# Performance work log

Measured on AMD Instinct MI355X. Metric: run time of the kernel, lower is better.

Reference implementation:

```python
import jax, jax.numpy as jnp
import numpy as np

N = 400000
CIN = 16
COUT = 32
K = 9  # taps in a (1,3,3) or (3,1,3) kernel
EPS = 1e-5


def subm_conv(feat, nbr, W):
    """Submanifold sparse conv as gather-matmul-scatter.
    feat: [N, C]; nbr: [N, K] indices in [0, N] (N == missing -> zero); W: [K, C, O].
    """
    feat_pad = jnp.concatenate([feat, jnp.zeros((1, feat.shape[1]), feat.dtype)], axis=0)
    g = feat_pad[nbr]                       # [N, K, C] irregular gather
    return jnp.einsum('nkc,kco->no', g, W)  # [N, O]


def bn_relu(x, gamma, beta, mean, var):
    # eval-mode BatchNorm1d over channel dim + ReLU
    return jax.nn.relu((x - mean) * jax.lax.rsqrt(var + EPS) * gamma + beta)


def setup_inputs() -> dict:
    key = jax.random.key(0)
    ks = jax.random.split(key, 8)
    features = jax.random.normal(ks[0], (N, CIN), jnp.float32)
    nbr13 = jax.random.randint(ks[1], (N, K), 0, N + 1, jnp.int32)
    nbr31 = jax.random.randint(ks[2], (N, K), 0, N + 1, jnp.int32)
    w1 = jax.random.normal(ks[3], (K, CIN, COUT), jnp.float32) * 0.05
    w12 = jax.random.normal(ks[4], (K, COUT, COUT), jnp.float32) * 0.05
    w2 = jax.random.normal(ks[5], (K, CIN, COUT), jnp.float32) * 0.05
    w3 = jax.random.normal(ks[6], (K, COUT, COUT), jnp.float32) * 0.05
    gamma = jax.random.uniform(ks[7], (4, COUT), jnp.float32, 0.5, 1.5)
    beta = jnp.zeros((4, COUT), jnp.float32)
    mean = jnp.zeros((4, COUT), jnp.float32)
    var = jnp.ones((4, COUT), jnp.float32)
    return dict(features=features, nbr13=nbr13, nbr31=nbr31,
                w1=w1, w12=w12, w2=w2, w3=w3,
                gamma=gamma, beta=beta, mean=mean, var=var)


def reference(features, nbr13, nbr31, w1, w12, w2, w3, gamma, beta, mean, var):
    # shortcut branch: conv1x3 -> BN -> ReLU -> conv3x1 -> BN -> ReLU
    sc = bn_relu(subm_conv(features, nbr13, w1), gamma[0], beta[0], mean[0], var[0])
    sc = bn_relu(subm_conv(sc, nbr31, w12), gamma[1], beta[1], mean[1], var[1])
    # main branch: conv3x1 -> BN -> ReLU -> conv1x3 -> BN -> ReLU
    out = bn_relu(subm_conv(features, nbr31, w2), gamma[2], beta[2], mean[2], var[2])
    out = bn_relu(subm_conv(out, nbr13, w3), gamma[3], beta[3], mean[3], var[3])
    return out + sc
```

## Files before the change

### kernel.cpp

```cpp
#include <hip/hip_runtime.h>

#define NPTS 400000
#define KTAPS 9
#define BN_EPS 1e-5f
#define NTILES (NPTS / 16)

typedef __attribute__((ext_vector_type(8))) short bf16x8;
typedef __attribute__((ext_vector_type(4))) float f32x4;

__device__ __forceinline__ unsigned short f2bf(float f) {
    union { float f; unsigned int i; } v; v.f = f;
    v.i += 0x7fffu + ((v.i >> 16) & 1u);
    return (unsigned short)(v.i >> 16);
}

__global__ __launch_bounds__(256) void cvt_feat(const float* __restrict__ feat,
                                                unsigned short* __restrict__ fb) {
    int n = blockIdx.x * 256 + threadIdx.x;
    if (n >= NPTS) return;
    const float4* p = reinterpret_cast<const float4*>(feat + (size_t)n * 16);
    float4 a = p[0], b = p[1], c = p[2], d = p[3];
    float v[16] = {a.x,a.y,a.z,a.w, b.x,b.y,b.z,b.w,
                   c.x,c.y,c.z,c.w, d.x,d.y,d.z,d.w};
    unsigned int pk[8];
    #pragma unroll
    for (int j = 0; j < 8; ++j)
        pk[j] = (unsigned int)f2bf(v[2*j]) | ((unsigned int)f2bf(v[2*j+1]) << 16);
    uint4* o = reinterpret_cast<uint4*>(fb + (size_t)n * 16);
    o[0] = make_uint4(pk[0], pk[1], pk[2], pk[3]);
    o[1] = make_uint4(pk[4], pk[5], pk[6], pk[7]);
}

__global__ __launch_bounds__(256) void pack_all(
    const float* __restrict__ w1, const float* __restrict__ w2,
    const float* __restrict__ w12, const float* __restrict__ w3,
    const float* __restrict__ gamma, const float* __restrict__ beta,
    const float* __restrict__ mean, const float* __restrict__ var,
    unsigned short* __restrict__ pw, float* __restrict__ sbf)
{
    int t = blockIdx.x * 256 + threadIdx.x;
    if (t < 28672) {
        const float* W; int CIN, f;
        if      (t < 5120)  { W = w1;  CIN = 16; f = t; }
        else if (t < 10240) { W = w2;  CIN = 16; f = t - 5120; }
        else if (t < 19456) { W = w12; CIN = 32; f = t - 10240; }
        else                { W = w3;  CIN = 32; f = t - 19456; }
        int j = f & 7, l = (f >> 3) & 63, fb = f >> 9;
        int g = fb >> 1, b = fb & 1;
        int kk = 8 * (l >> 4) + j;
        int tap, ch;
        if (CIN == 16) { tap = 2 * g + (kk >> 4); ch = kk & 15; }
        else           { tap = g;                 ch = kk;      }
        float w = (tap < KTAPS) ? W[((size_t)(tap * CIN + ch)) * 32 + b * 16 + (l & 15)] : 0.f;
        pw[t] = f2bf(w);
    } else if (t < 28672 + 128) {
        int r = t - 28672;
        float s  = gamma[r] * rsqrtf(var[r] + BN_EPS);
        float bb = beta[r] - mean[r] * s;
        sbf[2 * r]     = s;
        sbf[2 * r + 1] = bb;
    }
}

template<int CIN, bool ADD, bool OUT_BF16>
__global__ __launch_bounds__(256) void conv_mfma(
    const unsigned short* __restrict__ tab,
    const int* __restrict__ nbr,
    const float* __restrict__ Wf32,
    const unsigned short* __restrict__ pW,
    const float* __restrict__ sbf,
    const float* __restrict__ gam, const float* __restrict__ bet,
    const float* __restrict__ mea, const float* __restrict__ var,
    void* __restrict__ outp)
{
    constexpr int NFRAG = (CIN == 16) ? 5 : 9;
    __shared__ __align__(16) unsigned short Bp[NFRAG * 1024];
    __shared__ float2 SB[32];

    const int tid  = threadIdx.x;
    const int lane = tid & 63;
    const int lrow = lane & 15, lgrp = lane >> 4;
    const int tile = blockIdx.x * 4 + (tid >> 6);
    const int tb   = tile * 16;
    const int prow = tb + lrow;

    int idx[KTAPS];
    #pragma unroll
    for (int k = 0; k < KTAPS; ++k) idx[k] = nbr[(size_t)prow * KTAPS + k];

    if (pW != nullptr) {
        #pragma unroll
        for (int i = tid; i < NFRAG * 128; i += 256)
            reinterpret_cast<uint4*>(Bp)[i] = reinterpret_cast<const uint4*>(pW)[i];
        if (tid < 32) SB[tid] = reinterpret_cast<const float2*>(sbf)[tid];
    } else {
        for (int f = tid; f < NFRAG * 1024; f += 256) {
            int j = f & 7, l = (f >> 3) & 63, fb = f >> 9;
            int g = fb >> 1, b = fb & 1;
            int kk = 8 * (l >> 4) + j;
            int tap, ch;
            if (CIN == 16) { tap = 2 * g + (kk >> 4); ch = kk & 15; }
            else           { tap = g;                 ch = kk;      }
            float w = (tap < KTAPS) ? Wf32[((size_t)(tap * CIN + ch)) * 32 + b * 16 + (l & 15)] : 0.f;
            Bp[f] = f2bf(w);
        }
        if (tid < 32) {
            float s  = gam[tid] * rsqrtf(var[tid] + BN_EPS);
            float bb = bet[tid] - mea[tid] * s;
            SB[tid] = make_float2(s, bb);
        }
    }
    __syncthreads();

    uint4 ga[NFRAG];
    #pragma unroll
    for (int q = 0; q < NFRAG; ++q) {
        int tsel, boff;
        if (CIN == 16) { tsel = 2 * q + (lgrp >> 1); if (tsel > 8) tsel = 8;
                         boff = (lgrp & 1) * 16; }
        else           { tsel = q; boff = lgrp * 16; }
        int id = idx[tsel];
        int s = (id < NPTS) ? id : 0;
        uint4 gv = *reinterpret_cast<const uint4*>(
            reinterpret_cast<const char*>(tab) + (size_t)s * (CIN * 2) + boff);
        if (id >= NPTS) gv = make_uint4(0u, 0u, 0u, 0u);
        ga[q] = gv;
    }

    f32x4 acc0 = {0.f, 0.f, 0.f, 0.f}, acc1 = {0.f, 0.f, 0.f, 0.f};
    #pragma unroll
    for (int q = 0; q < NFRAG; ++q) {
        bf16x8 a  = *reinterpret_cast<const bf16x8*>(&ga[q]);
        bf16x8 b0 = *reinterpret_cast<const bf16x8*>(&Bp[(2*q + 0) * 512 + lane * 8]);
        bf16x8 b1 = *reinterpret_cast<const bf16x8*>(&Bp[(2*q + 1) * 512 + lane * 8]);
        acc0 = __builtin_amdgcn_mfma_f32_16x16x32_bf16(a, b0, acc0, 0, 0, 0);
        acc1 = __builtin_amdgcn_mfma_f32_16x16x32_bf16(a, b1, acc1, 0, 0, 0);
    }

    #pragma unroll
    for (int b = 0; b < 2; ++b) {
        const int o = b * 16 + lrow;
        const float2 sv = SB[o];
        const f32x4 a = (b == 0) ? acc0 : acc1;
        #pragma unroll
        for (int r = 0; r < 4; ++r) {
            const int m = tb + 4 * lgrp + r;
            float y = fmaxf(fmaf(a[r], sv.x, sv.y), 0.f);
            if (OUT_BF16) {
                ((unsigned short*)outp)[(size_t)m * 32 + o] = f2bf(y);
            } else {
                float* po = (float*)outp + (size_t)m * 32 + o;
                if (ADD) y += *po;
                *po = y;
            }
        }
    }
}

extern "C" void kernel_launch(void* const* d_in, const int* in_sizes, int n_in,
                              void* d_out, int out_size, void* d_ws, size_t ws_size,
                              hipStream_t stream) {
    const float* features = (const float*)d_in[0];
    const int*   nbr13    = (const int*)  d_in[1];
    const int*   nbr31    = (const int*)  d_in[2];
    const float* w1       = (const float*)d_in[3];
    const float* w12      = (const float*)d_in[4];
    const float* w2       = (const float*)d_in[5];
    const float* w3       = (const float*)d_in[6];
    const float* gamma    = (const float*)d_in[7];
    const float* beta     = (const float*)d_in[8];
    const float* mean     = (const float*)d_in[9];
    const float* var      = (const float*)d_in[10];
    float* out = (float*)d_out;

    const size_t tabShorts = (size_t)NPTS * 32;
    unsigned short* sc1 = (unsigned short*)d_ws;
    unsigned short* tmn = sc1 + tabShorts;
    unsigned short* fb  = (unsigned short*)d_out;

    unsigned short* pw  = nullptr;
    float*          sbf = nullptr;
    const size_t need = 2 * tabShorts * 2 + 28672 * 2 + 256 * 4;
    if (ws_size >= need) {
        pw  = tmn + tabShorts;
        sbf = (float*)(pw + 28672);
        pack_all<<<113, 256, 0, stream>>>(w1, w2, w12, w3, gamma, beta, mean, var, pw, sbf);
    }

    cvt_feat<<<(NPTS + 255) / 256, 256, 0, stream>>>(features, fb);

    const unsigned short* pw1  = pw;
    const unsigned short* pw2  = pw ? pw + 5120  : nullptr;
    const unsigned short* pw12 = pw ? pw + 10240 : nullptr;
    const unsigned short* pw3  = pw ? pw + 19456 : nullptr;

    dim3 grid(NTILES / 4), block(256);

    conv_mfma<16, false, true><<<grid, block, 0, stream>>>(
        fb, nbr13, w1, pw1, sbf ? sbf + 0 : nullptr,
        gamma + 0,  beta + 0,  mean + 0,  var + 0,  sc1);
    conv_mfma<16, false, true><<<grid, block, 0, stream>>>(
        fb, nbr31, w2, pw2, sbf ? sbf + 128 : nullptr,
        gamma + 64, beta + 64, mean + 64, var + 64, tmn);
    conv_mfma<32, false, false><<<grid, block, 0, stream>>>(
        tmn, nbr13, w3, pw3, sbf ? sbf + 192 : nullptr,
        gamma + 96, beta + 96, mean + 96, var + 96, out);
    conv_mfma<32, true, false><<<grid, block, 0, stream>>>(
        sc1, nbr31, w12, pw12, sbf ? sbf + 64 : nullptr,
        gamma + 32, beta + 32, mean + 32, var + 32, out);
}
```

Before: 262.6 us.

## Fuse paired convs into two kernels sharing neighbor loads and output write

Merges the two first-stage convolutions into one kernel that loads both neighbor tables once per tile and writes both bf16 intermediates. Merges the two second-stage convolutions into one kernel that computes both branches and writes the summed fp32 output once. This removes the read-modify-write of the output and two kernel launches. Each thread now holds twice as many gather registers and the kernels use more LDS, which may lower occupancy.

```diff
diff --git a/kernel.cpp b/kernel.cpp
--- a/kernel.cpp
+++ b/kernel.cpp
@@ -62,20 +62,39 @@
     }
 }
 
-template<int CIN, bool ADD, bool OUT_BF16>
-__global__ __launch_bounds__(256) void conv_mfma(
-    const unsigned short* __restrict__ tab,
-    const int* __restrict__ nbr,
-    const float* __restrict__ Wf32,
-    const unsigned short* __restrict__ pW,
-    const float* __restrict__ sbf,
-    const float* __restrict__ gam, const float* __restrict__ bet,
-    const float* __restrict__ mea, const float* __restrict__ var,
-    void* __restrict__ outp)
+__device__ __forceinline__ uint4 gather16(const char* __restrict__ base, int id,
+                                          int rowBytes, int boff) {
+    int s = (id < NPTS) ? id : 0;
+    uint4 v = *reinterpret_cast<const uint4*>(base + (size_t)s * rowBytes + boff);
+    if (id >= NPTS) v = make_uint4(0u, 0u, 0u, 0u);
+    return v;
+}
+
+__device__ __forceinline__ void pack_lds(unsigned short* Bp, const float* W,
+                                         int CIN, int nshorts, int tid) {
+    for (int f = tid; f < nshorts; f += 256) {
+        int j = f & 7, l = (f >> 3) & 63, fb = f >> 9;
+        int g = fb >> 1, b = fb & 1;
+        int kk = 8 * (l >> 4) + j;
+        int tap, ch;
+        if (CIN == 16) { tap = 2 * g + (kk >> 4); ch = kk & 15; }
+        else           { tap = g;                 ch = kk;      }
+        float w = (tap < KTAPS) ? W[((size_t)(tap * CIN + ch)) * 32 + b * 16 + (l & 15)] : 0.f;
+        Bp[f] = f2bf(w);
+    }
+}
+
+__global__ __launch_bounds__(256) void convA(
+    const unsigned short* __restrict__ fb,
+    const int* __restrict__ nbr13, const int* __restrict__ nbr31,
+    const float* __restrict__ w1f, const float* __restrict__ w2f,
+    const unsigned short* __restrict__ pW, const float* __restrict__ sbf,
+    const float* __restrict__ gamma, const float* __restrict__ beta,
+    const float* __restrict__ mean, const float* __restrict__ var,
+    unsigned short* __restrict__ sc1, unsigned short* __restrict__ tmn)
 {
-    constexpr int NFRAG = (CIN == 16) ? 5 : 9;
-    __shared__ __align__(16) unsigned short Bp[NFRAG * 1024];
-    __shared__ float2 SB[32];
+    __shared__ __align__(16) unsigned short Bp[10240];
+    __shared__ float2 SB[64];
 
     const int tid  = threadIdx.x;
     const int lane = tid & 63;
@@ -84,75 +103,149 @@
     const int tb   = tile * 16;
     const int prow = tb + lrow;
 
-    int idx[KTAPS];
-    #pragma unroll
-    for (int k = 0; k < KTAPS; ++k) idx[k] = nbr[(size_t)prow * KTAPS + k];
+    int i13[KTAPS], i31[KTAPS];
+    #pragma unroll
+    for (int k = 0; k < KTAPS; ++k) i13[k] = nbr13[(size_t)prow * KTAPS + k];
+    #pragma unroll
+    for (int k = 0; k < KTAPS; ++k) i31[k] = nbr31[(size_t)prow * KTAPS + k];
 
     if (pW != nullptr) {
         #pragma unroll
-        for (int i = tid; i < NFRAG * 128; i += 256)
+        for (int i = tid; i < 1280; i += 256)
             reinterpret_cast<uint4*>(Bp)[i] = reinterpret_cast<const uint4*>(pW)[i];
-        if (tid < 32) SB[tid] = reinterpret_cast<const float2*>(sbf)[tid];
+        if (tid < 64)
+            SB[tid] = reinterpret_cast<const float2*>(sbf)[(tid < 32) ? tid : tid + 32];
     } else {
-        for (int f = tid; f < NFRAG * 1024; f += 256) {
-            int j = f & 7, l = (f >> 3) & 63, fb = f >> 9;
-            int g = fb >> 1, b = fb & 1;
-            int kk = 8 * (l >> 4) + j;
-            int tap, ch;
-            if (CIN == 16) { tap = 2 * g + (kk >> 4); ch = kk & 15; }
-            else           { tap = g;                 ch = kk;      }
-            float w = (tap < KTAPS) ? Wf32[((size_t)(tap * CIN + ch)) * 32 + b * 16 + (l & 15)] : 0.f;
-            Bp[f] = f2bf(w);
-        }
-        if (tid < 32) {
-            float s  = gam[tid] * rsqrtf(var[tid] + BN_EPS);
-            float bb = bet[tid] - mea[tid] * s;
+        pack_lds(Bp, w1f, 16, 5120, tid);
+        pack_lds(Bp + 5120, w2f, 16, 5120, tid);
+        if (tid < 64) {
+            int row = (tid < 32) ? 0 : 2, o = tid & 31;
+            float s  = gamma[row*32+o] * rsqrtf(var[row*32+o] + BN_EPS);
+            float bb = beta[row*32+o] - mean[row*32+o] * s;
             SB[tid] = make_float2(s, bb);
         }
     }
     __syncthreads();
 
-    uint4 ga[NFRAG];
-    #pragma unroll
-    for (int q = 0; q < NFRAG; ++q) {
-        int tsel, boff;
-        if (CIN == 16) { tsel = 2 * q + (lgrp >> 1); if (tsel > 8) tsel = 8;
-                         boff = (lgrp & 1) * 16; }
-        else           { tsel = q; boff = lgrp * 16; }
-        int id = idx[tsel];
-        int s = (id < NPTS) ? id : 0;
-        uint4 gv = *reinterpret_cast<const uint4*>(
-            reinterpret_cast<const char*>(tab) + (size_t)s * (CIN * 2) + boff);
-        if (id >= NPTS) gv = make_uint4(0u, 0u, 0u, 0u);
-        ga[q] = gv;
-    }
-
-    f32x4 acc0 = {0.f, 0.f, 0.f, 0.f}, acc1 = {0.f, 0.f, 0.f, 0.f};
-    #pragma unroll
-    for (int q = 0; q < NFRAG; ++q) {
-        bf16x8 a  = *reinterpret_cast<const bf16x8*>(&ga[q]);
-        bf16x8 b0 = *reinterpret_cast<const bf16x8*>(&Bp[(2*q + 0) * 512 + lane * 8]);
-        bf16x8 b1 = *reinterpret_cast<const bf16x8*>(&Bp[(2*q + 1) * 512 + lane * 8]);
-        acc0 = __builtin_amdgcn_mfma_f32_16x16x32_bf16(a, b0, acc0, 0, 0, 0);
-        acc1 = __builtin_amdgcn_mfma_f32_16x16x32_bf16(a, b1, acc1, 0, 0, 0);
+    uint4 g1[5], g2[5];
+    #pragma unroll
+    for (int q = 0; q < 5; ++q) {
+        int tsel = 2 * q + (lgrp >> 1); if (tsel > 8) tsel = 8;
+        int boff = (lgrp & 1) * 16;
+        g1[q] = gather16((const char*)fb, i13[tsel], 32, boff);
+        g2[q] = gather16((const char*)fb, i31[tsel], 32, boff);
+    }
+
+    f32x4 a10 = {0,0,0,0}, a11 = {0,0,0,0}, a20 = {0,0,0,0}, a21 = {0,0,0,0};
+    #pragma unroll
+    for (int q = 0; q < 5; ++q) {
+        bf16x8 x1 = *reinterpret_cast<const bf16x8*>(&g1[q]);
+        bf16x8 x2 = *reinterpret_cast<const bf16x8*>(&g2[q]);
+        bf16x8 b10 = *reinterpret_cast<const bf16x8*>(&Bp[(2*q+0)*512 + lane*8]);
+        bf16x8 b11 = *reinterpret_cast<const bf16x8*>(&Bp[(2*q+1)*512 + lane*8]);
+        bf16x8 b20 = *reinterpret_cast<const bf16x8*>(&Bp[5120 + (2*q+0)*512 + lane*8]);
+        bf16x8 b21 = *reinterpret_cast<const bf16x8*>(&Bp[5120 + (2*q+1)*512 + lane*8]);
+        a10 = __builtin_amdgcn_mfma_f32_16x16x32_bf16(x1, b10, a10, 0, 0, 0);
+        a11 = __builtin_amdgcn_mfma_f32_16x16x32_bf16(x1, b11, a11, 0, 0, 0);
+        a20 = __builtin_amdgcn_mfma_f32_16x16x32_bf16(x2, b20, a20, 0, 0, 0);
+        a21 = __builtin_amdgcn_mfma_f32_16x16x32_bf16(x2, b21, a21, 0, 0, 0);
     }
 
     #pragma unroll
     for (int b = 0; b < 2; ++b) {
         const int o = b * 16 + lrow;
-        const float2 sv = SB[o];
-        const f32x4 a = (b == 0) ? acc0 : acc1;
+        const float2 s0 = SB[o];
+        const float2 s2 = SB[32 + o];
+        const f32x4 v1 = (b == 0) ? a10 : a11;
+        const f32x4 v2 = (b == 0) ? a20 : a21;
         #pragma unroll
         for (int r = 0; r < 4; ++r) {
             const int m = tb + 4 * lgrp + r;
-            float y = fmaxf(fmaf(a[r], sv.x, sv.y), 0.f);
-            if (OUT_BF16) {
-                ((unsigned short*)outp)[(size_t)m * 32 + o] = f2bf(y);
-            } else {
-                float* po = (float*)outp + (size_t)m * 32 + o;
-                if (ADD) y += *po;
-                *po = y;
-            }
+            sc1[(size_t)m * 32 + o] = f2bf(fmaxf(fmaf(v1[r], s0.x, s0.y), 0.f));
+            tmn[(size_t)m * 32 + o] = f2bf(fmaxf(fmaf(v2[r], s2.x, s2.y), 0.f));
+        }
+    }
+}
+
+__global__ __launch_bounds__(256) void convB(
+    const unsigned short* __restrict__ sc1, const unsigned short* __restrict__ tmn,
+    const int* __restrict__ nbr13, const int* __restrict__ nbr31,
+    const float* __restrict__ w12f, const float* __restrict__ w3f,
+    const unsigned short* __restrict__ pW, const float* __restrict__ sbf,
+    const float* __restrict__ gamma, const float* __restrict__ beta,
+    const float* __restrict__ mean, const float* __restrict__ var,
+    float* __restrict__ out)
+{
+    __shared__ __align__(16) unsigned short Bp[18432];
+    __shared__ float2 SB[64];
+
+    const int tid  = threadIdx.x;
+    const int lane = tid & 63;
+    const int lrow = lane & 15, lgrp = lane >> 4;
+    const int tile = blockIdx.x * 4 + (tid >> 6);
+    const int tb   = tile * 16;
+    const int prow = tb + lrow;
+
+    int i13[KTAPS], i31[KTAPS];
+    #pragma unroll
+    for (int k = 0; k < KTAPS; ++k) i13[k] = nbr13[(size_t)prow * KTAPS + k];
+    #pragma unroll
+    for (int k = 0; k < KTAPS; ++k) i31[k] = nbr31[(size_t)prow * KTAPS + k];
+
+    if (pW != nullptr) {
+        #pragma unroll
+        for (int i = tid; i < 2304; i += 256)
+            reinterpret_cast<uint4*>(Bp)[i] =
+                reinterpret_cast<const uint4*>(pW + 10240)[i];
+        if (tid < 64)
+            SB[tid] = reinterpret_cast<const float2*>(sbf)[32 + ((tid < 32) ? tid : tid + 32)];
+    } else {
+        pack_lds(Bp, w12f, 32, 9216, tid);
+        pack_lds(Bp + 9216, w3f, 32, 9216, tid);
+        if (tid < 64) {
+            int row = (tid < 32) ? 1 : 3, o = tid & 31;
+            float s  = gamma[row*32+o] * rsqrtf(var[row*32+o] + BN_EPS);
+            float bb = beta[row*32+o] - mean[row*32+o] * s;
+            SB[tid] = make_float2(s, bb);
+        }
+    }
+    __syncthreads();
+
+    const int boff = lgrp * 16;
+    uint4 gs[KTAPS], gt[KTAPS];
+    #pragma unroll
+    for (int q = 0; q < KTAPS; ++q) gs[q] = gather16((const char*)sc1, i31[q], 64, boff);
+    #pragma unroll
+    for (int q = 0; q < KTAPS; ++q) gt[q] = gather16((const char*)tmn, i13[q], 64, boff);
+
+    f32x4 s0 = {0,0,0,0}, s1 = {0,0,0,0}, t0 = {0,0,0,0}, t1 = {0,0,0,0};
+    #pragma unroll
+    for (int q = 0; q < KTAPS; ++q) {
+        bf16x8 xs = *reinterpret_cast<const bf16x8*>(&gs[q]);
+        bf16x8 xt = *reinterpret_cast<const bf16x8*>(&gt[q]);
+        bf16x8 bs0 = *reinterpret_cast<const bf16x8*>(&Bp[(2*q+0)*512 + lane*8]);
+        bf16x8 bs1 = *reinterpret_cast<const bf16x8*>(&Bp[(2*q+1)*512 + lane*8]);
+        bf16x8 bt0 = *reinterpret_cast<const bf16x8*>(&Bp[9216 + (2*q+0)*512 + lane*8]);
+        bf16x8 bt1 = *reinterpret_cast<const bf16x8*>(&Bp[9216 + (2*q+1)*512 + lane*8]);
+        s0 = __builtin_amdgcn_mfma_f32_16x16x32_bf16(xs, bs0, s0, 0, 0, 0);
+        s1 = __builtin_amdgcn_mfma_f32_16x16x32_bf16(xs, bs1, s1, 0, 0, 0);
+        t0 = __builtin_amdgcn_mfma_f32_16x16x32_bf16(xt, bt0, t0, 0, 0, 0);
+        t1 = __builtin_amdgcn_mfma_f32_16x16x32_bf16(xt, bt1, t1, 0, 0, 0);
+    }
+
+    #pragma unroll
+    for (int b = 0; b < 2; ++b) {
+        const int o = b * 16 + lrow;
+        const float2 c1 = SB[o];
+        const float2 c3 = SB[32 + o];
+        const f32x4 vs = (b == 0) ? s0 : s1;
+        const f32x4 vt = (b == 0) ? t0 : t1;
+        #pragma unroll
+        for (int r = 0; r < 4; ++r) {
+            const int m = tb + 4 * lgrp + r;
+            float ys = fmaxf(fmaf(vs[r], c1.x, c1.y), 0.f);
+            float yt = fmaxf(fmaf(vt[r], c3.x, c3.y), 0.f);
+            out[(size_t)m * 32 + o] = ys + yt;
         }
     }
 }
@@ -189,23 +282,10 @@
 
     cvt_feat<<<(NPTS + 255) / 256, 256, 0, stream>>>(features, fb);
 
-    const unsigned short* pw1  = pw;
-    const unsigned short* pw2  = pw ? pw + 5120  : nullptr;
-    const unsigned short* pw12 = pw ? pw + 10240 : nullptr;
-    const unsigned short* pw3  = pw ? pw + 19456 : nullptr;
-
     dim3 grid(NTILES / 4), block(256);
 
-    conv_mfma<16, false, true><<<grid, block, 0, stream>>>(
-        fb, nbr13, w1, pw1, sbf ? sbf + 0 : nullptr,
-        gamma + 0,  beta + 0,  mean + 0,  var + 0,  sc1);
-    conv_mfma<16, false, true><<<grid, block, 0, stream>>>(
-        fb, nbr31, w2, pw2, sbf ? sbf + 128 : nullptr,
-        gamma + 64, beta + 64, mean + 64, var + 64, tmn);
-    conv_mfma<32, false, false><<<grid, block, 0, stream>>>(
-        tmn, nbr13, w3, pw3, sbf ? sbf + 192 : nullptr,
-        gamma + 96, beta + 96, mean + 96, var + 96, out);
-    conv_mfma<32, true, false><<<grid, block, 0, stream>>>(
-        sc1, nbr31, w12, pw12, sbf ? sbf + 64 : nullptr,
-        gamma + 32, beta + 32, mean + 32, var + 32, out);
-}
+    convA<<<grid, block, 0, stream>>>(fb, nbr13, nbr31, w1, w2, pw, sbf,
+                                      gamma, beta, mean, var, sc1, tmn);
+    convB<<<grid, block, 0, stream>>>(sc1, tmn, nbr13, nbr31, w12, w3, pw, sbf,
+                                      gamma, beta, mean, var, out);
+}
```

Result: faster. 251.3 us (-4.3%).
